# Performance work log

Measured on AMD Instinct MI355X. Metric: run time of the kernel, lower is better.

Reference implementation:

```python
import jax, jax.numpy as jnp
import numpy as np

N_NODES = 100000
N_EDGES = 1600000
IN_FEATS = 128
OUT_FEATS = 64
NUM_HEADS = 1
K_HOPS = 3
NEG_SLOPE = 0.2


def setup_inputs() -> dict:
    key = jax.random.key(0)
    kf, kw, kl, kr, ks, kd = jax.random.split(key, 6)
    feat = jax.random.normal(kf, (N_NODES, IN_FEATS), dtype=jnp.float32)
    # xavier-normal-ish scaling (gain for relu ~ sqrt(2))
    W = jax.random.normal(kw, (OUT_FEATS * NUM_HEADS, IN_FEATS), dtype=jnp.float32) * np.sqrt(2.0 / (IN_FEATS + OUT_FEATS * NUM_HEADS))
    attn_l = jax.random.normal(kl, (1, NUM_HEADS, OUT_FEATS), dtype=jnp.float32) * 0.1
    attn_r = jax.random.normal(kr, (1, NUM_HEADS, OUT_FEATS), dtype=jnp.float32) * 0.1
    src = jax.random.randint(ks, (N_EDGES,), 0, N_NODES, dtype=jnp.int32)
    dst = jax.random.randint(kd, (N_EDGES,), 0, N_NODES, dtype=jnp.int32)
    return {"feat": feat, "W": W, "attn_l": attn_l, "attn_r": attn_r, "src": src, "dst": dst}


def _edge_softmax(e, dst, n_nodes):
    # e: [E, H, 1]; softmax over incoming edges of each dst node
    emax = jax.ops.segment_max(e, dst, num_segments=n_nodes)  # [N, H, 1]
    ee = jnp.exp(e - emax[dst])
    denom = jax.ops.segment_sum(ee, dst, num_segments=n_nodes)
    return ee / denom[dst]


def reference(feat, W, attn_l, attn_r, src, dst):
    n = feat.shape[0]
    h = (feat @ W.T).reshape(n, NUM_HEADS, OUT_FEATS)  # [N, H, F]
    el = jnp.sum(h * attn_l, axis=-1, keepdims=True)   # [N, H, 1]
    er = jnp.sum(h * attn_r, axis=-1, keepdims=True)   # [N, H, 1]
    e = el[src] + er[dst]                               # [E, H, 1]
    e = jnp.where(e > 0, e, NEG_SLOPE * e)              # leaky_relu
    a = _edge_softmax(e, dst, n)                        # [E, H, 1]

    ones = jnp.ones((src.shape[0],), dtype=feat.dtype)
    out_deg = jax.ops.segment_sum(ones, src, num_segments=n)
    in_deg = jax.ops.segment_sum(ones, dst, num_segments=n)
    out_norm = jnp.power(jnp.clip(out_deg, 1.0, None), -0.5)[:, None, None]  # deg^-0.5
    in_norm = jnp.power(jnp.clip(in_deg, 1.0, None), 0.5)[:, None, None]     # deg^+0.5 (as in source)

    feat_src = h
    for _ in range(K_HOPS):
        feat_src = feat_src * out_norm
        m = feat_src[src] * a                            # [E, H, F]
        feat_src = jax.ops.segment_sum(m, dst, num_segments=n)
        feat_src = feat_src * in_norm
    return feat_src  # [N, H, F]
```

## Files before the change

kernel.cpp:

```cpp
#include <hip/hip_runtime.h>
#include <hip/hip_fp16.h>
#include <math.h>

#define N_NODES 100000
#define N_EDGES 1600000
#define IN_F 128
#define OUT_F 64
#define NEG_SLOPE 0.2f

#define NBUCK 391
#define PB 512
#define EPB (N_EDGES / PB)

#define FS 132

typedef __attribute__((ext_vector_type(8))) short short8;
typedef __attribute__((ext_vector_type(4))) float f32x4;

__device__ __forceinline__ unsigned pack_bf(float f) {
    unsigned u  = __float_as_uint(f);
    unsigned hi = u & 0xffff0000u;
    float    lo = f - __uint_as_float(hi);
    return hi | (__float_as_uint(lo) >> 16);
}

__device__ __forceinline__ void unpack8(uint4 p0, uint4 p1, short8& hi, short8& lo) {
    hi[0] = (short)(p0.x >> 16); lo[0] = (short)(p0.x & 0xffffu);
    hi[1] = (short)(p0.y >> 16); lo[1] = (short)(p0.y & 0xffffu);
    hi[2] = (short)(p0.z >> 16); lo[2] = (short)(p0.z & 0xffffu);
    hi[3] = (short)(p0.w >> 16); lo[3] = (short)(p0.w & 0xffffu);
    hi[4] = (short)(p1.x >> 16); lo[4] = (short)(p1.x & 0xffffu);
    hi[5] = (short)(p1.y >> 16); lo[5] = (short)(p1.y & 0xffffu);
    hi[6] = (short)(p1.z >> 16); lo[6] = (short)(p1.z & 0xffffu);
    hi[7] = (short)(p1.w >> 16); lo[7] = (short)(p1.w & 0xffffu);
}

__global__ __launch_bounds__(256) void k_gemm(
        const float* __restrict__ feat, const float* __restrict__ W,
        const float* __restrict__ attn_l, const float* __restrict__ attn_r,
        __half* __restrict__ h16, float* __restrict__ el, float* __restrict__ er) {
    __shared__ __align__(16) unsigned flds[64 * FS];
    __shared__ __align__(16) unsigned wlds[64 * FS];
    int t = threadIdx.x;
    int n0 = blockIdx.x * 64;

    #pragma unroll
    for (int j = 0; j < 8; ++j) {
        int idx = t + j * 256;
        int row = idx >> 5, k4 = (idx & 31) * 4;
        float4 wv = *(const float4*)&W[row * IN_F + k4];
        unsigned* wp = &wlds[row * FS + k4];
        wp[0] = pack_bf(wv.x); wp[1] = pack_bf(wv.y);
        wp[2] = pack_bf(wv.z); wp[3] = pack_bf(wv.w);
        int g = n0 + row;
        float4 fv = {0.f, 0.f, 0.f, 0.f};
        if (g < N_NODES) fv = *(const float4*)&feat[(size_t)g * IN_F + k4];
        unsigned* fp = &flds[row * FS + k4];
        fp[0] = pack_bf(fv.x); fp[1] = pack_bf(fv.y);
        fp[2] = pack_bf(fv.z); fp[3] = pack_bf(fv.w);
    }
    __syncthreads();

    int lane = t & 63, wv_ = t >> 6;
    int quad = lane >> 4, nl = lane & 15;
    int mrow = wv_ * 16 + nl;

    f32x4 acc[4];
    #pragma unroll
    for (int nt = 0; nt < 4; ++nt) acc[nt] = (f32x4){0.f, 0.f, 0.f, 0.f};

    #pragma unroll
    for (int ks = 0; ks < 4; ++ks) {
        int ko = ks * 32 + quad * 8;
        const uint4* ap = (const uint4*)&flds[mrow * FS + ko];
        uint4 a0 = ap[0], a1 = ap[1];
        short8 ahi, alo; unpack8(a0, a1, ahi, alo);
        #pragma unroll
        for (int nt = 0; nt < 4; ++nt) {
            const uint4* bp = (const uint4*)&wlds[(nt * 16 + nl) * FS + ko];
            uint4 b0 = bp[0], b1 = bp[1];
            short8 bhi, blo; unpack8(b0, b1, bhi, blo);
            acc[nt] = __builtin_amdgcn_mfma_f32_16x16x32_bf16(ahi, bhi, acc[nt], 0, 0, 0);
            acc[nt] = __builtin_amdgcn_mfma_f32_16x16x32_bf16(ahi, blo, acc[nt], 0, 0, 0);
            acc[nt] = __builtin_amdgcn_mfma_f32_16x16x32_bf16(alo, bhi, acc[nt], 0, 0, 0);
        }
    }

    float al4[4], ar4[4];
    #pragma unroll
    for (int nt = 0; nt < 4; ++nt) { al4[nt] = attn_l[nt * 16 + nl]; ar4[nt] = attn_r[nt * 16 + nl]; }
    float elp[4] = {0.f, 0.f, 0.f, 0.f}, erp[4] = {0.f, 0.f, 0.f, 0.f};
    #pragma unroll
    for (int nt = 0; nt < 4; ++nt)
        #pragma unroll
        for (int r = 0; r < 4; ++r) {
            elp[r] += acc[nt][r] * al4[nt];
            erp[r] += acc[nt][r] * ar4[nt];
        }
    #pragma unroll
    for (int off = 1; off <= 8; off <<= 1)
        #pragma unroll
        for (int r = 0; r < 4; ++r) {
            elp[r] += __shfl_xor(elp[r], off);
            erp[r] += __shfl_xor(erp[r], off);
        }
    int gbase = n0 + wv_ * 16 + quad * 4;
    if (nl == 0) {
        #pragma unroll
        for (int r = 0; r < 4; ++r) {
            int g = gbase + r;
            if (g < N_NODES) { el[g] = elp[r]; er[g] = erp[r]; }
        }
    }
    #pragma unroll
    for (int r = 0; r < 4; ++r) {
        int g = gbase + r;
        if (g < N_NODES) {
            #pragma unroll
            for (int nt = 0; nt < 4; ++nt)
                h16[(size_t)g * OUT_F + nt * 16 + nl] = __float2half(acc[nt][r]);
        }
    }
}

__global__ __launch_bounds__(256) void k_hist(
        const int* __restrict__ src, const int* __restrict__ dst,
        int* __restrict__ cntd, int* __restrict__ cnts) {
    __shared__ int hd[NBUCK], hs[NBUCK];
    int t = threadIdx.x, b = blockIdx.x;
    for (int k = t; k < NBUCK; k += 256) { hd[k] = 0; hs[k] = 0; }
    __syncthreads();
    int base = b * EPB;
    for (int i = t; i < EPB; i += 256) {
        atomicAdd(&hd[dst[base + i] >> 8], 1);
        atomicAdd(&hs[src[base + i] >> 8], 1);
    }
    __syncthreads();
    for (int k = t; k < NBUCK; k += 256) {
        cntd[k * PB + b] = hd[k];
        cnts[k * PB + b] = hs[k];
    }
}

__global__ __launch_bounds__(256) void k_colsum(const int* __restrict__ cntd,
                                                const int* __restrict__ cnts,
                                                int* __restrict__ totd,
                                                int* __restrict__ tots) {
    __shared__ int s[256];
    int b = blockIdx.x, t = threadIdx.x;
    const int* m; int* o; int k;
    if (b < NBUCK) { m = cntd; o = totd; k = b; }
    else           { m = cnts; o = tots; k = b - NBUCK; }
    s[t] = m[k * PB + t] + m[k * PB + t + 256];
    __syncthreads();
    for (int d = 128; d; d >>= 1) { if (t < d) s[t] += s[t + d]; __syncthreads(); }
    if (t == 0) o[k] = s[0];
}

__global__ __launch_bounds__(512) void k_bstart(const int* __restrict__ totd,
                                                const int* __restrict__ tots,
                                                int* bstartd, int* bstarts) {
    __shared__ int s[512];
    int t = threadIdx.x;
    int v = (t < NBUCK) ? totd[t] : 0;
    s[t] = v; __syncthreads();
    for (int d = 1; d < 512; d <<= 1) { int a = (t >= d) ? s[t - d] : 0; __syncthreads(); s[t] += a; __syncthreads(); }
    if (t <= NBUCK) bstartd[t] = s[t] - v;
    __syncthreads();
    int v2 = (t < NBUCK) ? tots[t] : 0;
    s[t] = v2; __syncthreads();
    for (int d = 1; d < 512; d <<= 1) { int a = (t >= d) ? s[t - d] : 0; __syncthreads(); s[t] += a; __syncthreads(); }
    if (t <= NBUCK) bstarts[t] = s[t] - v2;
}

__global__ __launch_bounds__(512) void k_blockoff(const int* __restrict__ bstartd,
                                                  const int* __restrict__ bstarts,
                                                  int* cntd, int* cnts) {
    __shared__ int s[512];
    int b = blockIdx.x, t = threadIdx.x;
    int* m; const int* bs; int k;
    if (b < NBUCK) { m = cntd; bs = bstartd; k = b; }
    else           { m = cnts; bs = bstarts; k = b - NBUCK; }
    int c = m[k * PB + t];
    s[t] = c; __syncthreads();
    for (int d = 1; d < 512; d <<= 1) { int a = (t >= d) ? s[t - d] : 0; __syncthreads(); s[t] += a; __syncthreads(); }
    m[k * PB + t] = bs[k] + s[t] - c;
}

__global__ __launch_bounds__(256) void k_scatter3(
        const int* __restrict__ src, const int* __restrict__ dst,
        const float* __restrict__ el, const float* __restrict__ er,
        const int* __restrict__ offd, const int* __restrict__ offs,
        int2* __restrict__ tmpd, unsigned char* __restrict__ tmps) {
    __shared__ int lOffD[NBUCK], lFillD[NBUCK];
    __shared__ int lOffS[NBUCK], lFillS[NBUCK];
    int t = threadIdx.x, b = blockIdx.x;
    for (int k = t; k < NBUCK; k += 256) {
        lOffD[k] = offd[k * PB + b]; lFillD[k] = 0;
        lOffS[k] = offs[k * PB + b]; lFillS[k] = 0;
    }
    __syncthreads();
    int base = b * EPB;
    for (int i = t; i < EPB; i += 256) {
        int e = base + i;
        int sN = src[e], d = dst[e];
        int ks = sN >> 8;
        int rs = atomicAdd(&lFillS[ks], 1);
        tmps[lOffS[ks] + rs] = (unsigned char)(sN & 255);
        float v = el[sN] + er[d];
        v = (v > 0.f) ? v : NEG_SLOPE * v;
        float pe = __expf(v);
        int kd = d >> 8;
        int rd = atomicAdd(&lFillD[kd], 1);
        int2 rec; rec.x = sN | ((d & 255) << 17); rec.y = __float_as_int(pe);
        tmpd[lOffD[kd] + rd] = rec;
    }
}

__global__ __launch_bounds__(256) void k_srccnt(
        const unsigned char* __restrict__ tmps, const int* __restrict__ bstarts,
        float* __restrict__ onorm) {
    __shared__ int cnt[256];
    int k = blockIdx.x, t = threadIdx.x;
    cnt[t] = 0; __syncthreads();
    int base = bstarts[k], end = bstarts[k + 1];
    for (int i = base + t; i < end; i += 256)
        atomicAdd(&cnt[tmps[i]], 1);
    __syncthreads();
    int idx = k * 256 + t;
    if (idx < N_NODES) onorm[idx] = rsqrtf((float)max(cnt[t], 1));
}

__global__ __launch_bounds__(256) void k_bucket(
        const int2* __restrict__ tmp, const int* __restrict__ bstart,
        const float* __restrict__ onorm, float2* __restrict__ csr,
        int* __restrict__ rowstart, float* __restrict__ sigma) {
    __shared__ int   cs[256];
    __shared__ int   excl[256];
    __shared__ int   fill[256];
    __shared__ float dsum[256];
    int k = blockIdx.x, t = threadIdx.x;
    int base = bstart[k], end = bstart[k + 1];
    cs[t] = 0; fill[t] = 0; dsum[t] = 0.f;
    __syncthreads();
    for (int i = base + t; i < end; i += 256)
        atomicAdd(&cs[(tmp[i].x >> 17) & 255], 1);
    __syncthreads();
    int c = cs[t];
    for (int d = 1; d < 256; d <<= 1) {
        int a = (t >= d) ? cs[t - d] : 0;
        __syncthreads();
        cs[t] += a;
        __syncthreads();
    }
    excl[t] = cs[t] - c;
    __syncthreads();
    int idx = k * 256 + t;
    if (idx <= N_NODES) rowstart[idx] = base + excl[t];
    for (int i = base + t; i < end; i += 256) {
        int2 rec = tmp[i];
        int dlow = (rec.x >> 17) & 255;
        int r = atomicAdd(&fill[dlow], 1);
        float pe = __int_as_float(rec.y);
        int sN = rec.x & 131071;
        float2 w;
        w.x = __int_as_float(sN);
        w.y = pe * onorm[sN];
        csr[base + excl[dlow] + r] = w;
        atomicAdd(&dsum[dlow], pe);
    }
    __syncthreads();
    if (idx < N_NODES) {
        float inn = sqrtf((float)max(c, 1));
        sigma[idx] = (c > 0) ? inn / dsum[t] : 0.f;
    }
}

template<typename OT>
__global__ __launch_bounds__(256) void k_spmm(
        const __half* __restrict__ x, const int* __restrict__ rowstart,
        const float2* __restrict__ csr, const float* __restrict__ sigma,
        OT* __restrict__ y) {
    int node = blockIdx.x * 32 + (threadIdx.x >> 3);
    int fl = threadIdx.x & 7;
    if (node >= N_NODES) return;
    int b = rowstart[node], e = rowstart[node + 1];
    float4 a0lo = {0.f, 0.f, 0.f, 0.f}, a0hi = {0.f, 0.f, 0.f, 0.f};
    float4 a1lo = {0.f, 0.f, 0.f, 0.f}, a1hi = {0.f, 0.f, 0.f, 0.f};
    for (int i = b; i < e; i += 8) {
        #pragma unroll
        for (int u = 0; u < 8; ++u) {
            int j = i + u;
            int jc = (j < e) ? j : (e - 1);
            float2 w = csr[jc];
            float vv = (j < e) ? w.y : 0.f;
            unsigned boff = ((unsigned)__float_as_int(w.x) << 7) | ((unsigned)fl << 4);
            uint4 pk = *(const uint4*)((const char*)x + boff);
            float2 f0 = __half22float2(*(__half2*)&pk.x);
            float2 f1 = __half22float2(*(__half2*)&pk.y);
            float2 f2 = __half22float2(*(__half2*)&pk.z);
            float2 f3 = __half22float2(*(__half2*)&pk.w);
            float4& alo = (u & 1) ? a1lo : a0lo;
            float4& ahi = (u & 1) ? a1hi : a0hi;
            alo.x += vv * f0.x; alo.y += vv * f0.y; alo.z += vv * f1.x; alo.w += vv * f1.y;
            ahi.x += vv * f2.x; ahi.y += vv * f2.y; ahi.z += vv * f3.x; ahi.w += vv * f3.y;
        }
    }
    float sg = sigma[node];
    float4 rlo, rhi;
    rlo.x = sg * (a0lo.x + a1lo.x); rlo.y = sg * (a0lo.y + a1lo.y);
    rlo.z = sg * (a0lo.z + a1lo.z); rlo.w = sg * (a0lo.w + a1lo.w);
    rhi.x = sg * (a0hi.x + a1hi.x); rhi.y = sg * (a0hi.y + a1hi.y);
    rhi.z = sg * (a0hi.z + a1hi.z); rhi.w = sg * (a0hi.w + a1hi.w);
    if constexpr (sizeof(OT) == 4) {
        float* yp = (float*)y + (size_t)node * OUT_F + fl * 8;
        *(float4*)yp       = rlo;
        *(float4*)(yp + 4) = rhi;
    } else {
        __half2 p0 = __floats2half2_rn(rlo.x, rlo.y);
        __half2 p1 = __floats2half2_rn(rlo.z, rlo.w);
        __half2 p2 = __floats2half2_rn(rhi.x, rhi.y);
        __half2 p3 = __floats2half2_rn(rhi.z, rhi.w);
        uint4 o;
        o.x = *(unsigned*)&p0; o.y = *(unsigned*)&p1;
        o.z = *(unsigned*)&p2; o.w = *(unsigned*)&p3;
        *(uint4*)((__half*)y + (size_t)node * OUT_F + fl * 8) = o;
    }
}

extern "C" void kernel_launch(void* const* d_in, const int* in_sizes, int n_in,
                              void* d_out, int out_size, void* d_ws, size_t ws_size,
                              hipStream_t stream) {
    const float* feat   = (const float*)d_in[0];
    const float* W      = (const float*)d_in[1];
    const float* attn_l = (const float*)d_in[2];
    const float* attn_r = (const float*)d_in[3];
    const int*   src    = (const int*)d_in[4];
    const int*   dst    = (const int*)d_in[5];
    float* out = (float*)d_out;

    char* p = (char*)d_ws;
    auto alloc = [&](size_t bytes) {
        void* r = (void*)p;
        p += (bytes + 255) & ~(size_t)255;
        return r;
    };
    __half* hbuf = (__half*)alloc((size_t)N_NODES * OUT_F * 2);
    char* r2 = (char*)alloc((size_t)N_EDGES * 8 + (size_t)N_EDGES);
    int2*  tmpd = (int2*)r2;
    unsigned char* tmps = (unsigned char*)(r2 + (size_t)N_EDGES * 8);
    __half* A   = (__half*)r2;

    float2* csr      = (float2*)alloc((size_t)N_EDGES * 8);
    int*    cntd     = (int*)   alloc((size_t)NBUCK * PB * 4);
    int*    cnts     = (int*)   alloc((size_t)NBUCK * PB * 4);
    int*    totd     = (int*)   alloc(NBUCK * 4);
    int*    tots     = (int*)   alloc(NBUCK * 4);
    int*    bstartd  = (int*)   alloc((NBUCK + 1) * 4);
    int*    bstarts  = (int*)   alloc((NBUCK + 1) * 4);
    int*    rowstart = (int*)   alloc((N_NODES + 1) * 4);
    float*  onorm    = (float*) alloc(N_NODES * 4);
    float*  sigma    = (float*) alloc(N_NODES * 4);
    float*  el       = (float*) alloc(N_NODES * 4);
    float*  er       = (float*) alloc(N_NODES * 4);

    const int NGB = (N_NODES + 63) / 64;

    k_gemm     <<<NGB,       256, 0, stream>>>(feat, W, attn_l, attn_r, hbuf, el, er);
    k_hist     <<<PB,        256, 0, stream>>>(src, dst, cntd, cnts);
    k_colsum   <<<2 * NBUCK, 256, 0, stream>>>(cntd, cnts, totd, tots);
    k_bstart   <<<1,         512, 0, stream>>>(totd, tots, bstartd, bstarts);
    k_blockoff <<<2 * NBUCK, 512, 0, stream>>>(bstartd, bstarts, cntd, cnts);
    k_scatter3 <<<PB,        256, 0, stream>>>(src, dst, el, er, cntd, cnts, tmpd, tmps);
    k_srccnt   <<<NBUCK,     256, 0, stream>>>(tmps, bstarts, onorm);
    k_bucket   <<<NBUCK,     256, 0, stream>>>(tmpd, bstartd, onorm, csr, rowstart, sigma);

    const int nb_spmm = (N_NODES + 31) / 32;
    k_spmm<__half><<<nb_spmm, 256, 0, stream>>>(hbuf, rowstart, csr, sigma, A);
    k_spmm<__half><<<nb_spmm, 256, 0, stream>>>(A,    rowstart, csr, sigma, hbuf);
    k_spmm<float> <<<nb_spmm, 256, 0, stream>>>(hbuf, rowstart, csr, sigma, out);
}
```

Measured before the change: 300.4 us.

## Stage scatter and bucket outputs in shared memory for coalesced global writes

The scatter kernel first builds a per-block bucket histogram and prefix sum, then sorts its edges locally in LDS. It writes them out contiguously per bucket, using a binary search over the prefix sums so global stores are coalesced rather than random. The bucket kernel likewise stages CSR entries in LDS when the bucket fits in BCAP and then copies them out linearly. The cost is extra passes over src/dst, more LDS use (EPB int2 plus bytes, about 28KB, and a 40KB stC array), and likely lower occupancy.

```diff
diff --git a/kernel.cpp b/kernel.cpp
--- a/kernel.cpp
+++ b/kernel.cpp
@@ -13,6 +13,7 @@
 #define EPB (N_EDGES / PB)
 
 #define FS 132
+#define BCAP 5120
 
 typedef __attribute__((ext_vector_type(8))) short short8;
 typedef __attribute__((ext_vector_type(4))) float f32x4;
@@ -192,28 +193,74 @@
         const float* __restrict__ el, const float* __restrict__ er,
         const int* __restrict__ offd, const int* __restrict__ offs,
         int2* __restrict__ tmpd, unsigned char* __restrict__ tmps) {
-    __shared__ int lOffD[NBUCK], lFillD[NBUCK];
-    __shared__ int lOffS[NBUCK], lFillS[NBUCK];
+    __shared__ int gOffD[NBUCK], gOffS[NBUCK];
+    __shared__ int hD[NBUCK], hS[NBUCK];
+    __shared__ int fD[NBUCK], fS[NBUCK];
+    __shared__ int sD[512], sS[512];
+    __shared__ int2 stD[EPB];
+    __shared__ unsigned char stS[EPB];
     int t = threadIdx.x, b = blockIdx.x;
     for (int k = t; k < NBUCK; k += 256) {
-        lOffD[k] = offd[k * PB + b]; lFillD[k] = 0;
-        lOffS[k] = offs[k * PB + b]; lFillS[k] = 0;
+        gOffD[k] = offd[k * PB + b]; gOffS[k] = offs[k * PB + b];
+        hD[k] = 0; hS[k] = 0; fD[k] = 0; fS[k] = 0;
     }
     __syncthreads();
     int base = b * EPB;
     for (int i = t; i < EPB; i += 256) {
+        atomicAdd(&hD[dst[base + i] >> 8], 1);
+        atomicAdd(&hS[src[base + i] >> 8], 1);
+    }
+    __syncthreads();
+    sD[t]       = (t < NBUCK) ? hD[t] : 0;
+    sD[t + 256] = (t + 256 < NBUCK) ? hD[t + 256] : 0;
+    sS[t]       = (t < NBUCK) ? hS[t] : 0;
+    sS[t + 256] = (t + 256 < NBUCK) ? hS[t + 256] : 0;
+    __syncthreads();
+    for (int d = 1; d < 512; d <<= 1) {
+        int a0 = (t >= d) ? sD[t - d] : 0;
+        int a1 = sD[t + 256 - d];
+        int b0 = (t >= d) ? sS[t - d] : 0;
+        int b1 = sS[t + 256 - d];
+        __syncthreads();
+        sD[t] += a0; sD[t + 256] += a1;
+        sS[t] += b0; sS[t + 256] += b1;
+        __syncthreads();
+    }
+    for (int k = t; k < NBUCK; k += 256) {
+        hD[k] = sD[k] - hD[k];
+        hS[k] = sS[k] - hS[k];
+    }
+    __syncthreads();
+    for (int i = t; i < EPB; i += 256) {
         int e = base + i;
-        int sN = src[e], d = dst[e];
+        int sN = src[e], dN = dst[e];
         int ks = sN >> 8;
-        int rs = atomicAdd(&lFillS[ks], 1);
-        tmps[lOffS[ks] + rs] = (unsigned char)(sN & 255);
-        float v = el[sN] + er[d];
+        int rs = atomicAdd(&fS[ks], 1);
+        stS[hS[ks] + rs] = (unsigned char)(sN & 255);
+        float v = el[sN] + er[dN];
         v = (v > 0.f) ? v : NEG_SLOPE * v;
         float pe = __expf(v);
-        int kd = d >> 8;
-        int rd = atomicAdd(&lFillD[kd], 1);
-        int2 rec; rec.x = sN | ((d & 255) << 17); rec.y = __float_as_int(pe);
-        tmpd[lOffD[kd] + rd] = rec;
+        int kd = dN >> 8;
+        int rd = atomicAdd(&fD[kd], 1);
+        int2 rec; rec.x = sN | ((dN & 255) << 17); rec.y = __float_as_int(pe);
+        stD[hD[kd] + rd] = rec;
+    }
+    __syncthreads();
+    for (int j = t; j < EPB; j += 256) {
+        int k = 0;
+        #pragma unroll
+        for (int step = 256; step > 0; step >>= 1) {
+            int c = k + step;
+            if (c <= 511 && sD[c - 1] <= j) k = c;
+        }
+        tmpd[gOffD[k] + (j - hD[k])] = stD[j];
+        int k2 = 0;
+        #pragma unroll
+        for (int step = 256; step > 0; step >>= 1) {
+            int c = k2 + step;
+            if (c <= 511 && sS[c - 1] <= j) k2 = c;
+        }
+        tmps[gOffS[k2] + (j - hS[k2])] = stS[j];
     }
 }
 
@@ -239,8 +286,11 @@
     __shared__ int   excl[256];
     __shared__ int   fill[256];
     __shared__ float dsum[256];
+    __shared__ float2 stC[BCAP];
     int k = blockIdx.x, t = threadIdx.x;
     int base = bstart[k], end = bstart[k + 1];
+    int tot = end - base;
+    bool staged = (tot <= BCAP);
     cs[t] = 0; fill[t] = 0; dsum[t] = 0.f;
     __syncthreads();
     for (int i = base + t; i < end; i += 256)
@@ -266,10 +316,15 @@
         float2 w;
         w.x = __int_as_float(sN);
         w.y = pe * onorm[sN];
-        csr[base + excl[dlow] + r] = w;
+        int pos = excl[dlow] + r;
+        if (staged) stC[pos] = w;
+        else        csr[base + pos] = w;
         atomicAdd(&dsum[dlow], pe);
     }
     __syncthreads();
+    if (staged)
+        for (int j = t; j < tot; j += 256)
+            csr[base + j] = stC[j];
     if (idx < N_NODES) {
         float inn = sqrtf((float)max(c, 1));
         sigma[idx] = (c > 0) ? inn / dsum[t] : 0.f;
```

Measured after the change: 290.1 us. -3.4%, faster.
